# Performance work log

Measured on AMD Instinct MI355X. Metric: run time of the kernel, lower is better.

The kernel has to match this reference:

```python
import jax, jax.numpy as jnp
import numpy as np

B, L, D, H = 2, 2048, 1024, 16
DH = D // H  # per-head dim = 64


def setup_inputs() -> dict:
    key = jax.random.key(0)
    ks = jax.random.split(key, 7)
    s = 1.0 / np.sqrt(D)
    x = jax.random.normal(ks[0], (B, L, D), dtype=jnp.float32)
    Wq = jax.random.normal(ks[1], (D, D), dtype=jnp.float32) * s
    bq = jax.random.normal(ks[2], (D,), dtype=jnp.float32) * s
    Wk = jax.random.normal(ks[3], (D, D), dtype=jnp.float32) * s
    bk = jax.random.normal(ks[4], (D,), dtype=jnp.float32) * s
    Wv = jax.random.normal(ks[5], (D, D), dtype=jnp.float32) * s
    bv = jax.random.normal(ks[6], (D,), dtype=jnp.float32) * s
    # strict upper-triangular causal mask; mask==1 means position is masked (-inf)
    atten_mask = jnp.triu(jnp.ones((L, L), dtype=jnp.int32), k=1)
    return {"x": x, "atten_mask": atten_mask, "Wq": Wq, "bq": bq,
            "Wk": Wk, "bk": bk, "Wv": Wv, "bv": bv}


def reference(x, atten_mask, Wq, bq, Wk, bk, Wv, bv):
    # nn.Linear: y = x @ W^T + b
    q = x @ Wq.T + bq  # [B,L,D]
    k = x @ Wk.T + bk
    v = x @ Wv.T + bv
    # contiguous split into heads == reshape to [B,L,H,DH]
    q = q.reshape(B, L, H, DH)
    k = k.reshape(B, L, H, DH)
    v = v.reshape(B, L, H, DH)
    scale = jnp.sqrt(jnp.float32(DH))
    scores = jnp.einsum('blhd,bmhd->bhlm', q, k) / scale  # [B,H,L,L]
    # torch.where(mask == 1, -inf, scores)
    scores = jnp.where(atten_mask[None, None] == 1, -jnp.inf, scores)
    attn = jax.nn.softmax(scores, axis=-1)
    out = jnp.einsum('bhlm,bmhd->blhd', attn, v)  # [B,L,H,DH]
    return out.reshape(B, L, D)  # concat heads along channel dim
```

## Files before the change

kernel.cpp:

```cpp
#include <hip/hip_runtime.h>
#include <hip/hip_bf16.h>

#define BDIM 2
#define LSEQ 2048
#define DMODEL 1024
#define NH 16
#define DHEAD 64
#define CTS 136

typedef __bf16 bf16_t;
typedef __attribute__((ext_vector_type(8))) __bf16 bf16x8;
typedef __attribute__((ext_vector_type(4))) __bf16 bf16x4;
typedef __attribute__((ext_vector_type(2))) __bf16 bf16x2;
typedef __attribute__((ext_vector_type(4))) float f32x4;
typedef __attribute__((ext_vector_type(4))) int i32x4;

static __device__ __forceinline__ f32x4 mfma16(bf16x8 a, bf16x8 b, f32x4 c) {
    return __builtin_amdgcn_mfma_f32_16x16x32_bf16(a, b, c, 0, 0, 0);
}

static __device__ __forceinline__ void load_lds16(const bf16_t* g, void* l) {
    __builtin_amdgcn_global_load_lds(
        (const __attribute__((address_space(1))) void*)g,
        (__attribute__((address_space(3))) void*)l, 16, 0, 0);
}

__global__ void convert_all(
    const float* __restrict__ x,
    const float* __restrict__ Wq, const float* __restrict__ Wk, const float* __restrict__ Wv,
    const float* __restrict__ bq, const float* __restrict__ bk, const float* __restrict__ bv,
    bf16_t* __restrict__ cx,
    bf16_t* __restrict__ cWq, bf16_t* __restrict__ cWk, bf16_t* __restrict__ cWv,
    bf16_t* __restrict__ cbq, bf16_t* __restrict__ cbk, bf16_t* __restrict__ cbv,
    float SQ)
{
    const int blk = blockIdx.x;
    const float* src; bf16_t* dst; int base, cnt; float sc = 1.0f;
    if (blk < 1024)      { src = x;  dst = cx;  base = blk * 1024;          cnt = 1024; }
    else if (blk < 1280) { src = Wq; dst = cWq; base = (blk - 1024) * 1024; cnt = 1024; sc = SQ; }
    else if (blk < 1536) { src = Wk; dst = cWk; base = (blk - 1280) * 1024; cnt = 1024; }
    else if (blk < 1792) { src = Wv; dst = cWv; base = (blk - 1536) * 1024; cnt = 1024; }
    else if (blk == 1792){ src = bq; dst = cbq; base = 0; cnt = 256; sc = SQ; }
    else if (blk == 1793){ src = bk; dst = cbk; base = 0; cnt = 256; }
    else                 { src = bv; dst = cbv; base = 0; cnt = 256; }

    for (int i = base + threadIdx.x; i < base + cnt; i += 256) {
        f32x4 v = *(const f32x4*)(src + 4 * (size_t)i);
        bf16x4 o;
        o[0] = (bf16_t)(v[0] * sc); o[1] = (bf16_t)(v[1] * sc);
        o[2] = (bf16_t)(v[2] * sc); o[3] = (bf16_t)(v[3] * sc);
        *(bf16x4*)(dst + 4 * (size_t)i) = o;
    }
}

__global__ __launch_bounds__(256) void qkv_gemm(
    const bf16_t* __restrict__ x,
    const bf16_t* __restrict__ W0, const bf16_t* __restrict__ W1, const bf16_t* __restrict__ W2,
    const bf16_t* __restrict__ b0, const bf16_t* __restrict__ b1, const bf16_t* __restrict__ b2,
    bf16_t* __restrict__ yq, bf16_t* __restrict__ yk, bf16_t* __restrict__ yvT)
{
    __shared__ alignas(16) char smem[128 * CTS * 2];
    bf16_t* At = (bf16_t*)smem;
    bf16_t* Bt = At + 128 * 64;
    bf16_t* Ct = (bf16_t*)smem;

    const int tid  = threadIdx.x;
    const int lane = tid & 63;
    const int w    = tid >> 6;
    const int quad = lane >> 4;
    const int n16  = lane & 15;
    const int lane3 = lane >> 3;
    const int lane7 = lane & 7;
    const int swz8  = (lane7 ^ lane3) * 8;

    const int m0 = blockIdx.y * 128;
    const int n0 = blockIdx.x * 128;
    const int z  = blockIdx.z;

    const bf16_t* W    = (z == 0) ? W0 : ((z == 1) ? W1 : W2);
    const bf16_t* bias = (z == 0) ? b0 : ((z == 1) ? b1 : b2);

    const int wm = (w >> 1) * 64;
    const int wn = (w & 1) * 64;

    f32x4 acc[4][4] = {};

    const bf16_t* gx = x + (size_t)(m0 + 32 * w + lane3) * DMODEL + swz8;
    const bf16_t* gw = W + (size_t)(n0 + 32 * w + lane3) * DMODEL + swz8;
    char* lA = (char*)At + w * 4096;
    char* lB = (char*)Bt + w * 4096;

    const int swz = n16 & 7;

    for (int k0 = 0; k0 < DMODEL; k0 += 64) {
        #pragma unroll
        for (int ii = 0; ii < 4; ++ii) {
            load_lds16(gx + (size_t)(8 * ii) * DMODEL + k0, lA + ii * 1024);
            load_lds16(gw + (size_t)(8 * ii) * DMODEL + k0, lB + ii * 1024);
        }
        __syncthreads();

        #pragma unroll
        for (int kk = 0; kk < 2; ++kk) {
            bf16x8 af[4], bfv[4];
            #pragma unroll
            for (int mt = 0; mt < 4; ++mt) {
                const bf16_t* ar = At + (wm + mt * 16 + n16) * 64;
                af[mt] = *(const bf16x8*)(ar + (((quad + 4 * kk)) ^ swz) * 8);
            }
            #pragma unroll
            for (int nt = 0; nt < 4; ++nt) {
                const bf16_t* br = Bt + (wn + nt * 16 + n16) * 64;
                bfv[nt] = *(const bf16x8*)(br + (((quad + 4 * kk)) ^ swz) * 8);
            }
            #pragma unroll
            for (int mt = 0; mt < 4; ++mt)
                #pragma unroll
                for (int nt = 0; nt < 4; ++nt)
                    acc[mt][nt] = mfma16(af[mt], bfv[nt], acc[mt][nt]);
        }
        __syncthreads();
    }

    if (z < 2) {
        bf16_t* y = (z == 0) ? yq : yk;
        #pragma unroll
        for (int nt = 0; nt < 4; ++nt) {
            int jc = wn + nt * 16 + n16;
            float bv = (float)bias[n0 + jc];
            #pragma unroll
            for (int mt = 0; mt < 4; ++mt) {
                int rr = wm + mt * 16 + quad * 4;
                #pragma unroll
                for (int r = 0; r < 4; ++r)
                    Ct[(rr + r) * CTS + jc] = (bf16_t)(acc[mt][nt][r] + bv);
            }
        }
        __syncthreads();
        const int l    = tid >> 1;
        const int half = tid & 1;
        const int hh   = (n0 >> 6) + half;
        const int i    = m0 + l;
        const int bb   = i >> 11, ll = i & 2047;
        bf16_t* dst = &y[(((size_t)bb * NH + hh) * LSEQ + ll) * DHEAD];
        const bf16_t* srcr = &Ct[l * CTS + half * 64];
        #pragma unroll
        for (int c = 0; c < 8; ++c)
            *(bf16x8*)(dst + c * 8) = *(const bf16x8*)(srcr + c * 8);
    } else {
        #pragma unroll
        for (int nt = 0; nt < 4; ++nt) {
            int j = n0 + wn + nt * 16 + n16;
            float bv = (float)bias[j];
            #pragma unroll
            for (int mt = 0; mt < 4; ++mt) {
                int i0 = m0 + wm + mt * 16 + quad * 4;
                int bb = i0 >> 11, l = i0 & 2047;
                bf16x4 pk;
                #pragma unroll
                for (int r = 0; r < 4; ++r) pk[r] = (bf16_t)(acc[mt][nt][r] + bv);
                *(bf16x4*)(&yvT[((size_t)bb * DMODEL + j) * LSEQ + l]) = pk;
            }
        }
    }
}

__global__ __launch_bounds__(256) void attn_fused(
    const bf16_t* __restrict__ qp,
    const bf16_t* __restrict__ kp,
    const bf16_t* __restrict__ vtp,
    float* __restrict__ out,
    float* __restrict__ Opart,
    float* __restrict__ ml)
{
    __shared__ alignas(16) bf16_t Ks[2][64 * 64];
    __shared__ alignas(16) bf16_t Vs[2][64 * 64];

    const int tid  = threadIdx.x;
    const int lane = tid & 63;
    const int w    = tid >> 6;
    const int quad = lane >> 4;
    const int n16  = lane & 15;
    const int lane3 = lane >> 3;
    const int lane7 = lane & 7;
    const int swz8  = (lane7 ^ lane3) * 8;
    const int swz   = n16 & 7;

    const int bh  = blockIdx.x;
    const int yy  = blockIdx.y;
    const int p   = yy & 7;
    const bool isA = (yy < 8);
    const int b = bh >> 4, h = bh & 15;
    const size_t hb = (size_t)bh * (LSEQ * DHEAD);

    float l_[2];
    f32x4 oacc[2][4];

    auto process = [&](int qt, int t0, int ntiles, bool maskTail) {
        int iqg[2];
        bf16x8 qb[2][2];
        #pragma unroll
        for (int g = 0; g < 2; ++g) {
            iqg[g] = qt * 128 + 32 * w + 16 * g + n16;
            const bf16_t* qq = qp + hb + (size_t)iqg[g] * DHEAD;
            qb[g][0] = *(const bf16x8*)(qq + quad * 8);
            qb[g][1] = *(const bf16x8*)(qq + 32 + quad * 8);
        }

        const bf16_t* gk = kp  + hb + (size_t)(t0 * 64 + 16 * w + lane3) * DHEAD + swz8;
        const bf16_t* gv = vtp + hb + (size_t)(16 * w + lane3) * LSEQ + t0 * 64 + swz8;

        int buf = 0;
        {
            char* lk = (char*)&Ks[0][0] + w * 2048;
            char* lv = (char*)&Vs[0][0] + w * 2048;
            load_lds16(gk,             lk);
            load_lds16(gk + 8 * DHEAD, lk + 1024);
            load_lds16(gv,             lv);
            load_lds16(gv + 8 * LSEQ,  lv + 1024);
            gk += 64 * DHEAD; gv += 64;
        }
        __syncthreads();

        for (int it = 0; it < ntiles; ++it) {
            if (it + 1 < ntiles) {
                char* lk = (char*)&Ks[buf ^ 1][0] + w * 2048;
                char* lv = (char*)&Vs[buf ^ 1][0] + w * 2048;
                load_lds16(gk,             lk);
                load_lds16(gk + 8 * DHEAD, lk + 1024);
                load_lds16(gv,             lv);
                load_lds16(gv + 8 * LSEQ,  lv + 1024);
                gk += 64 * DHEAD; gv += 64;
            }

            const bf16_t* kb = &Ks[buf][0];
            f32x4 s[2][4];
            #pragma unroll
            for (int t = 0; t < 4; ++t) {
                const bf16_t* krow = kb + (t * 16 + n16) * 64;
                bf16x8 k0v = *(const bf16x8*)(krow + ((quad    ) ^ swz) * 8);
                bf16x8 k1v = *(const bf16x8*)(krow + ((quad + 4) ^ swz) * 8);
                #pragma unroll
                for (int g = 0; g < 2; ++g) {
                    f32x4 z = {0.f, 0.f, 0.f, 0.f};
                    z = mfma16(k0v, qb[g][0], z);
                    z = mfma16(k1v, qb[g][1], z);
                    s[g][t] = z;
                }
            }

            if (maskTail && it >= ntiles - 2) {
                const int k0 = (t0 + it) * 64;
                #pragma unroll
                for (int g = 0; g < 2; ++g)
                    #pragma unroll
                    for (int t = 0; t < 4; ++t)
                        #pragma unroll
                        for (int r = 0; r < 4; ++r)
                            if (k0 + t * 16 + quad * 4 + r > iqg[g]) s[g][t][r] = -1e30f;
            }

            bf16x8 pb[2][2];
            #pragma unroll
            for (int g = 0; g < 2; ++g) {
                float rs = 0.f;
                int pr[4][2];
                #pragma unroll
                for (int t = 0; t < 4; ++t) {
                    float p0 = __builtin_amdgcn_exp2f(s[g][t][0]);
                    float p1 = __builtin_amdgcn_exp2f(s[g][t][1]);
                    float p2 = __builtin_amdgcn_exp2f(s[g][t][2]);
                    float p3 = __builtin_amdgcn_exp2f(s[g][t][3]);
                    rs += (p0 + p1) + (p2 + p3);
                    bf16x2 a; a[0] = (bf16_t)p0; a[1] = (bf16_t)p1;
                    bf16x2 c; c[0] = (bf16_t)p2; c[1] = (bf16_t)p3;
                    pr[t][0] = __builtin_bit_cast(int, a);
                    pr[t][1] = __builtin_bit_cast(int, c);
                }
                l_[g] += rs;

                #pragma unroll
                for (int c = 0; c < 2; ++c) {
                    int frag[4];
                    #pragma unroll
                    for (int pi = 0; pi < 4; ++pi) {
                        int srcl = ((((quad & 1) * 2) + (pi >> 1)) * 16 + n16) * 4;
                        int vA = __builtin_amdgcn_ds_bpermute(srcl, pr[2 * c][pi & 1]);
                        int vB = __builtin_amdgcn_ds_bpermute(srcl, pr[2 * c + 1][pi & 1]);
                        frag[pi] = (quad < 2) ? vA : vB;
                    }
                    i32x4 fv = {frag[0], frag[1], frag[2], frag[3]};
                    pb[g][c] = __builtin_bit_cast(bf16x8, fv);
                }
            }

            const bf16_t* vbs = &Vs[buf][0];
            #pragma unroll
            for (int c = 0; c < 2; ++c) {
                #pragma unroll
                for (int t = 0; t < 4; ++t) {
                    const bf16_t* vrow = vbs + (t * 16 + n16) * 64;
                    bf16x8 va = *(const bf16x8*)(vrow + ((quad + 4 * c) ^ swz) * 8);
                    oacc[0][t] = mfma16(va, pb[0][c], oacc[0][t]);
                    oacc[1][t] = mfma16(va, pb[1][c], oacc[1][t]);
                }
            }

            __syncthreads();
            buf ^= 1;
        }
    };

    auto zero_state = [&]() {
        #pragma unroll
        for (int g = 0; g < 2; ++g) {
            l_[g] = 0.f;
            #pragma unroll
            for (int t = 0; t < 4; ++t) { f32x4 zz = {0.f,0.f,0.f,0.f}; oacc[g][t] = zz; }
        }
    };

    auto store_partial = [&](int pidx) {
        #pragma unroll
        for (int g = 0; g < 2; ++g) {
            float ls = l_[g];
            ls += __shfl_xor(ls, 16, 64);
            ls += __shfl_xor(ls, 32, 64);
            const int row = 32 * w + 16 * g + n16;
            float* Ob = Opart + (size_t)pidx * (128 * 64) + row * 64;
            #pragma unroll
            for (int t = 0; t < 4; ++t)
                *(f32x4*)(Ob + t * 16 + quad * 4) = oacc[g][t];
            if (quad == 0) ml[(size_t)pidx * 128 + row] = ls;
        }
    };

    if (isA) {
        zero_state();
        process(p, 0, 2 * p + 2, true);
        #pragma unroll
        for (int g = 0; g < 2; ++g) {
            float ls = l_[g];
            ls += __shfl_xor(ls, 16, 64);
            ls += __shfl_xor(ls, 32, 64);
            const float inv = 1.0f / ls;
            const int iq = p * 128 + 32 * w + 16 * g + n16;
            float* orow = out + ((size_t)b * LSEQ + iq) * DMODEL + h * DHEAD;
            #pragma unroll
            for (int t = 0; t < 4; ++t) {
                f32x4 o;
                o[0] = oacc[g][t][0] * inv; o[1] = oacc[g][t][1] * inv;
                o[2] = oacc[g][t][2] * inv; o[3] = oacc[g][t][3] * inv;
                *(f32x4*)(orow + t * 16 + quad * 4) = o;
            }
        }
        zero_state();
        process(15 - p, 0, 15 - 2 * p, false);
        store_partial((bh * 8 + (7 - p)) * 2 + 0);
    } else {
        zero_state();
        process(15 - p, 15 - 2 * p, 17, true);
        store_partial((bh * 8 + (7 - p)) * 2 + 1);
    }
}

__global__ __launch_bounds__(256) void attn_combine(
    const float* __restrict__ Opart, const float* __restrict__ ml,
    float* __restrict__ out)
{
    const int bh = blockIdx.x;
    const int q8 = blockIdx.y;
    const int t  = threadIdx.x;
    const int row = t >> 1;
    const int dh0 = (t & 1) * 32;
    const int p0  = (bh * 8 + q8) * 2;
    const int b = bh >> 4, h = bh & 15;

    float l0 = ml[(size_t)p0 * 128 + row];
    float l1 = ml[(size_t)(p0 + 1) * 128 + row];
    float inv = 1.0f / (l0 + l1);

    const float* P0 = Opart + (size_t)p0 * (128 * 64) + row * 64 + dh0;
    const float* P1 = P0 + 128 * 64;
    float* orow = out + ((size_t)b * LSEQ + ((8 + q8) * 128 + row)) * DMODEL
                + h * DHEAD + dh0;
    #pragma unroll
    for (int c = 0; c < 8; ++c) {
        f32x4 o0 = *(const f32x4*)(P0 + 4 * c);
        f32x4 o1 = *(const f32x4*)(P1 + 4 * c);
        f32x4 o;
        o[0] = (o0[0] + o1[0]) * inv;
        o[1] = (o0[1] + o1[1]) * inv;
        o[2] = (o0[2] + o1[2]) * inv;
        o[3] = (o0[3] + o1[3]) * inv;
        *(f32x4*)(orow + 4 * c) = o;
    }
}

extern "C" void kernel_launch(void* const* d_in, const int* in_sizes, int n_in,
                              void* d_out, int out_size, void* d_ws, size_t ws_size,
                              hipStream_t stream)
{
    const float* x  = (const float*)d_in[0];
    const float* Wq = (const float*)d_in[2];
    const float* bq = (const float*)d_in[3];
    const float* Wk = (const float*)d_in[4];
    const float* bk = (const float*)d_in[5];
    const float* Wv = (const float*)d_in[6];
    const float* bv = (const float*)d_in[7];
    float* out = (float*)d_out;

    char* ws = (char*)d_ws;
    bf16_t* q   = (bf16_t*)(ws);
    bf16_t* k   = (bf16_t*)(ws + 8u  * 1024 * 1024);
    bf16_t* vT  = (bf16_t*)(ws + 16u * 1024 * 1024);
    bf16_t* cx  = (bf16_t*)(ws + 24u * 1024 * 1024);
    bf16_t* cWq = (bf16_t*)(ws + 32u * 1024 * 1024);
    bf16_t* cWk = (bf16_t*)(ws + 34u * 1024 * 1024);
    bf16_t* cWv = (bf16_t*)(ws + 36u * 1024 * 1024);
    bf16_t* cbq = (bf16_t*)(ws + 38u * 1024 * 1024);
    bf16_t* cbk = (bf16_t*)(ws + 38u * 1024 * 1024 + 4096);
    bf16_t* cbv = (bf16_t*)(ws + 38u * 1024 * 1024 + 8192);
    float*  mlp = (float*) (ws + 39u * 1024 * 1024);
    float*  Op  = (float*) (ws + 40u * 1024 * 1024);

    const float SQ = 0.125f * 1.44269504088896f;

    convert_all<<<1795, 256, 0, stream>>>(x, Wq, Wk, Wv, bq, bk, bv,
                                          cx, cWq, cWk, cWv, cbq, cbk, cbv, SQ);

    dim3 g1(DMODEL / 128, (BDIM * LSEQ) / 128, 3);
    qkv_gemm<<<g1, 256, 0, stream>>>(cx, cWq, cWk, cWv, cbq, cbk, cbv, q, k, vT);

    dim3 g2(BDIM * NH, 16, 1);
    attn_fused<<<g2, 256, 0, stream>>>(q, k, vT, out, Op, mlp);

    dim3 g3(BDIM * NH, 8, 1);
    attn_combine<<<g3, 256, 0, stream>>>(Op, mlp, out);
}
```

Baseline: 188.1 us.

## Rebalance causal attention into 30 table-driven split-KV jobs per head

Replaces the paired A/B block scheme (16 blocks per head, some running two passes) with a static job table of 30 blocks per head. Each block handles one query tile over a KV range of at most about 12 tiles, and longer query tiles are split into 2 or 3 partials. The combine kernel now sums a variable number of partials per query tile. The goal is shorter, more even per-block work and more blocks to fill the CUs. The cost is extra partial writes and reads and a moved workspace layout, where the Op buffer now overlaps the cx region.

```diff
diff --git a/kernel.cpp b/kernel.cpp
--- a/kernel.cpp
+++ b/kernel.cpp
@@ -173,6 +173,17 @@
     float* __restrict__ Opart,
     float* __restrict__ ml)
 {
+    static const short JQT[30] = {0,1,2,3,4,5, 6,6, 7,7, 8,8, 9,9, 10,10, 11,11,
+                                  12,12,12, 13,13,13, 14,14,14, 15,15,15};
+    static const short JT0[30] = {0,0,0,0,0,0, 0,7, 0,8, 0,9, 0,10, 0,11, 0,12,
+                                  0,9,18, 0,10,19, 0,10,20, 0,11,22};
+    static const short JNT[30] = {2,4,6,8,10,12, 7,7, 8,8, 9,9, 10,10, 11,11, 12,12,
+                                  9,9,8, 10,9,9, 10,10,10, 11,11,10};
+    static const short JPS[30] = {-1,-1,-1,-1,-1,-1, 0,1, 2,3, 4,5, 6,7, 8,9, 10,11,
+                                  12,13,14, 15,16,17, 18,19,20, 21,22,23};
+    static const short JMK[30] = {1,1,1,1,1,1, 0,1, 0,1, 0,1, 0,1, 0,1, 0,1,
+                                  0,0,1, 0,0,1, 0,0,1, 0,0,1};
+
     __shared__ alignas(16) bf16_t Ks[2][64 * 64];
     __shared__ alignas(16) bf16_t Vs[2][64 * 64];
 
@@ -187,140 +198,150 @@
     const int swz   = n16 & 7;
 
     const int bh  = blockIdx.x;
-    const int yy  = blockIdx.y;
-    const int p   = yy & 7;
-    const bool isA = (yy < 8);
+    const int job = blockIdx.y;
+    const int qt     = JQT[job];
+    const int t0     = JT0[job];
+    const int ntiles = JNT[job];
+    const int pslot  = JPS[job];
+    const bool maskTail = (JMK[job] != 0);
+
     const int b = bh >> 4, h = bh & 15;
     const size_t hb = (size_t)bh * (LSEQ * DHEAD);
 
-    float l_[2];
-    f32x4 oacc[2][4];
-
-    auto process = [&](int qt, int t0, int ntiles, bool maskTail) {
-        int iqg[2];
-        bf16x8 qb[2][2];
-        #pragma unroll
-        for (int g = 0; g < 2; ++g) {
-            iqg[g] = qt * 128 + 32 * w + 16 * g + n16;
-            const bf16_t* qq = qp + hb + (size_t)iqg[g] * DHEAD;
-            qb[g][0] = *(const bf16x8*)(qq + quad * 8);
-            qb[g][1] = *(const bf16x8*)(qq + 32 + quad * 8);
-        }
-
-        const bf16_t* gk = kp  + hb + (size_t)(t0 * 64 + 16 * w + lane3) * DHEAD + swz8;
-        const bf16_t* gv = vtp + hb + (size_t)(16 * w + lane3) * LSEQ + t0 * 64 + swz8;
-
-        int buf = 0;
-        {
-            char* lk = (char*)&Ks[0][0] + w * 2048;
-            char* lv = (char*)&Vs[0][0] + w * 2048;
+    float l_[2] = {0.f, 0.f};
+    f32x4 oacc[2][4] = {};
+
+    int iqg[2];
+    bf16x8 qb[2][2];
+    #pragma unroll
+    for (int g = 0; g < 2; ++g) {
+        iqg[g] = qt * 128 + 32 * w + 16 * g + n16;
+        const bf16_t* qq = qp + hb + (size_t)iqg[g] * DHEAD;
+        qb[g][0] = *(const bf16x8*)(qq + quad * 8);
+        qb[g][1] = *(const bf16x8*)(qq + 32 + quad * 8);
+    }
+
+    const bf16_t* gk = kp  + hb + (size_t)(t0 * 64 + 16 * w + lane3) * DHEAD + swz8;
+    const bf16_t* gv = vtp + hb + (size_t)(16 * w + lane3) * LSEQ + t0 * 64 + swz8;
+
+    int buf = 0;
+    {
+        char* lk = (char*)&Ks[0][0] + w * 2048;
+        char* lv = (char*)&Vs[0][0] + w * 2048;
+        load_lds16(gk,             lk);
+        load_lds16(gk + 8 * DHEAD, lk + 1024);
+        load_lds16(gv,             lv);
+        load_lds16(gv + 8 * LSEQ,  lv + 1024);
+        gk += 64 * DHEAD; gv += 64;
+    }
+    __syncthreads();
+
+    for (int it = 0; it < ntiles; ++it) {
+        if (it + 1 < ntiles) {
+            char* lk = (char*)&Ks[buf ^ 1][0] + w * 2048;
+            char* lv = (char*)&Vs[buf ^ 1][0] + w * 2048;
             load_lds16(gk,             lk);
             load_lds16(gk + 8 * DHEAD, lk + 1024);
             load_lds16(gv,             lv);
             load_lds16(gv + 8 * LSEQ,  lv + 1024);
             gk += 64 * DHEAD; gv += 64;
         }
+
+        const bf16_t* kb = &Ks[buf][0];
+        f32x4 s[2][4];
+        #pragma unroll
+        for (int t = 0; t < 4; ++t) {
+            const bf16_t* krow = kb + (t * 16 + n16) * 64;
+            bf16x8 k0v = *(const bf16x8*)(krow + ((quad    ) ^ swz) * 8);
+            bf16x8 k1v = *(const bf16x8*)(krow + ((quad + 4) ^ swz) * 8);
+            #pragma unroll
+            for (int g = 0; g < 2; ++g) {
+                f32x4 z = {0.f, 0.f, 0.f, 0.f};
+                z = mfma16(k0v, qb[g][0], z);
+                z = mfma16(k1v, qb[g][1], z);
+                s[g][t] = z;
+            }
+        }
+
+        if (maskTail && it >= ntiles - 2) {
+            const int k0 = (t0 + it) * 64;
+            #pragma unroll
+            for (int g = 0; g < 2; ++g)
+                #pragma unroll
+                for (int t = 0; t < 4; ++t)
+                    #pragma unroll
+                    for (int r = 0; r < 4; ++r)
+                        if (k0 + t * 16 + quad * 4 + r > iqg[g]) s[g][t][r] = -1e30f;
+        }
+
+        bf16x8 pb[2][2];
+        #pragma unroll
+        for (int g = 0; g < 2; ++g) {
+            float rs = 0.f;
+            int pr[4][2];
+            #pragma unroll
+            for (int t = 0; t < 4; ++t) {
+                float p0 = __builtin_amdgcn_exp2f(s[g][t][0]);
+                float p1 = __builtin_amdgcn_exp2f(s[g][t][1]);
+                float p2 = __builtin_amdgcn_exp2f(s[g][t][2]);
+                float p3 = __builtin_amdgcn_exp2f(s[g][t][3]);
+                rs += (p0 + p1) + (p2 + p3);
+                bf16x2 a; a[0] = (bf16_t)p0; a[1] = (bf16_t)p1;
+                bf16x2 c; c[0] = (bf16_t)p2; c[1] = (bf16_t)p3;
+                pr[t][0] = __builtin_bit_cast(int, a);
+                pr[t][1] = __builtin_bit_cast(int, c);
+            }
+            l_[g] += rs;
+
+            #pragma unroll
+            for (int c = 0; c < 2; ++c) {
+                int frag[4];
+                #pragma unroll
+                for (int pi = 0; pi < 4; ++pi) {
+                    int srcl = ((((quad & 1) * 2) + (pi >> 1)) * 16 + n16) * 4;
+                    int vA = __builtin_amdgcn_ds_bpermute(srcl, pr[2 * c][pi & 1]);
+                    int vB = __builtin_amdgcn_ds_bpermute(srcl, pr[2 * c + 1][pi & 1]);
+                    frag[pi] = (quad < 2) ? vA : vB;
+                }
+                i32x4 fv = {frag[0], frag[1], frag[2], frag[3]};
+                pb[g][c] = __builtin_bit_cast(bf16x8, fv);
+            }
+        }
+
+        const bf16_t* vbs = &Vs[buf][0];
+        #pragma unroll
+        for (int c = 0; c < 2; ++c) {
+            #pragma unroll
+            for (int t = 0; t < 4; ++t) {
+                const bf16_t* vrow = vbs + (t * 16 + n16) * 64;
+                bf16x8 va = *(const bf16x8*)(vrow + ((quad + 4 * c) ^ swz) * 8);
+                oacc[0][t] = mfma16(va, pb[0][c], oacc[0][t]);
+                oacc[1][t] = mfma16(va, pb[1][c], oacc[1][t]);
+            }
+        }
+
         __syncthreads();
-
-        for (int it = 0; it < ntiles; ++it) {
-            if (it + 1 < ntiles) {
-                char* lk = (char*)&Ks[buf ^ 1][0] + w * 2048;
-                char* lv = (char*)&Vs[buf ^ 1][0] + w * 2048;
-                load_lds16(gk,             lk);
-                load_lds16(gk + 8 * DHEAD, lk + 1024);
-                load_lds16(gv,             lv);
-                load_lds16(gv + 8 * LSEQ,  lv + 1024);
-                gk += 64 * DHEAD; gv += 64;
-            }
-
-            const bf16_t* kb = &Ks[buf][0];
-            f32x4 s[2][4];
+        buf ^= 1;
+    }
+
+    if (pslot < 0) {
+        #pragma unroll
+        for (int g = 0; g < 2; ++g) {
+            float ls = l_[g];
+            ls += __shfl_xor(ls, 16, 64);
+            ls += __shfl_xor(ls, 32, 64);
+            const float inv = 1.0f / ls;
+            float* orow = out + ((size_t)b * LSEQ + iqg[g]) * DMODEL + h * DHEAD;
             #pragma unroll
             for (int t = 0; t < 4; ++t) {
-                const bf16_t* krow = kb + (t * 16 + n16) * 64;
-                bf16x8 k0v = *(const bf16x8*)(krow + ((quad    ) ^ swz) * 8);
-                bf16x8 k1v = *(const bf16x8*)(krow + ((quad + 4) ^ swz) * 8);
-                #pragma unroll
-                for (int g = 0; g < 2; ++g) {
-                    f32x4 z = {0.f, 0.f, 0.f, 0.f};
-                    z = mfma16(k0v, qb[g][0], z);
-                    z = mfma16(k1v, qb[g][1], z);
-                    s[g][t] = z;
-                }
-            }
-
-            if (maskTail && it >= ntiles - 2) {
-                const int k0 = (t0 + it) * 64;
-                #pragma unroll
-                for (int g = 0; g < 2; ++g)
-                    #pragma unroll
-                    for (int t = 0; t < 4; ++t)
-                        #pragma unroll
-                        for (int r = 0; r < 4; ++r)
-                            if (k0 + t * 16 + quad * 4 + r > iqg[g]) s[g][t][r] = -1e30f;
-            }
-
-            bf16x8 pb[2][2];
-            #pragma unroll
-            for (int g = 0; g < 2; ++g) {
-                float rs = 0.f;
-                int pr[4][2];
-                #pragma unroll
-                for (int t = 0; t < 4; ++t) {
-                    float p0 = __builtin_amdgcn_exp2f(s[g][t][0]);
-                    float p1 = __builtin_amdgcn_exp2f(s[g][t][1]);
-                    float p2 = __builtin_amdgcn_exp2f(s[g][t][2]);
-                    float p3 = __builtin_amdgcn_exp2f(s[g][t][3]);
-                    rs += (p0 + p1) + (p2 + p3);
-                    bf16x2 a; a[0] = (bf16_t)p0; a[1] = (bf16_t)p1;
-                    bf16x2 c; c[0] = (bf16_t)p2; c[1] = (bf16_t)p3;
-                    pr[t][0] = __builtin_bit_cast(int, a);
-                    pr[t][1] = __builtin_bit_cast(int, c);
-                }
-                l_[g] += rs;
-
-                #pragma unroll
-                for (int c = 0; c < 2; ++c) {
-                    int frag[4];
-                    #pragma unroll
-                    for (int pi = 0; pi < 4; ++pi) {
-                        int srcl = ((((quad & 1) * 2) + (pi >> 1)) * 16 + n16) * 4;
-                        int vA = __builtin_amdgcn_ds_bpermute(srcl, pr[2 * c][pi & 1]);
-                        int vB = __builtin_amdgcn_ds_bpermute(srcl, pr[2 * c + 1][pi & 1]);
-                        frag[pi] = (quad < 2) ? vA : vB;
-                    }
-                    i32x4 fv = {frag[0], frag[1], frag[2], frag[3]};
-                    pb[g][c] = __builtin_bit_cast(bf16x8, fv);
-                }
-            }
-
-            const bf16_t* vbs = &Vs[buf][0];
-            #pragma unroll
-            for (int c = 0; c < 2; ++c) {
-                #pragma unroll
-                for (int t = 0; t < 4; ++t) {
-                    const bf16_t* vrow = vbs + (t * 16 + n16) * 64;
-                    bf16x8 va = *(const bf16x8*)(vrow + ((quad + 4 * c) ^ swz) * 8);
-                    oacc[0][t] = mfma16(va, pb[0][c], oacc[0][t]);
-                    oacc[1][t] = mfma16(va, pb[1][c], oacc[1][t]);
-                }
-            }
-
-            __syncthreads();
-            buf ^= 1;
-        }
-    };
-
-    auto zero_state = [&]() {
-        #pragma unroll
-        for (int g = 0; g < 2; ++g) {
-            l_[g] = 0.f;
-            #pragma unroll
-            for (int t = 0; t < 4; ++t) { f32x4 zz = {0.f,0.f,0.f,0.f}; oacc[g][t] = zz; }
-        }
-    };
-
-    auto store_partial = [&](int pidx) {
+                f32x4 o;
+                o[0] = oacc[g][t][0] * inv; o[1] = oacc[g][t][1] * inv;
+                o[2] = oacc[g][t][2] * inv; o[3] = oacc[g][t][3] * inv;
+                *(f32x4*)(orow + t * 16 + quad * 4) = o;
+            }
+        }
+    } else {
+        const int pidx = bh * 24 + pslot;
         #pragma unroll
         for (int g = 0; g < 2; ++g) {
             float ls = l_[g];
@@ -333,34 +354,6 @@
                 *(f32x4*)(Ob + t * 16 + quad * 4) = oacc[g][t];
             if (quad == 0) ml[(size_t)pidx * 128 + row] = ls;
         }
-    };
-
-    if (isA) {
-        zero_state();
-        process(p, 0, 2 * p + 2, true);
-        #pragma unroll
-        for (int g = 0; g < 2; ++g) {
-            float ls = l_[g];
-            ls += __shfl_xor(ls, 16, 64);
-            ls += __shfl_xor(ls, 32, 64);
-            const float inv = 1.0f / ls;
-            const int iq = p * 128 + 32 * w + 16 * g + n16;
-            float* orow = out + ((size_t)b * LSEQ + iq) * DMODEL + h * DHEAD;
-            #pragma unroll
-            for (int t = 0; t < 4; ++t) {
-                f32x4 o;
-                o[0] = oacc[g][t][0] * inv; o[1] = oacc[g][t][1] * inv;
-                o[2] = oacc[g][t][2] * inv; o[3] = oacc[g][t][3] * inv;
-                *(f32x4*)(orow + t * 16 + quad * 4) = o;
-            }
-        }
-        zero_state();
-        process(15 - p, 0, 15 - 2 * p, false);
-        store_partial((bh * 8 + (7 - p)) * 2 + 0);
-    } else {
-        zero_state();
-        process(15 - p, 15 - 2 * p, 17, true);
-        store_partial((bh * 8 + (7 - p)) * 2 + 1);
     }
 }
 
@@ -368,31 +361,35 @@
     const float* __restrict__ Opart, const float* __restrict__ ml,
     float* __restrict__ out)
 {
+    static const short PB[10] = {0,2,4,6,8,10, 12,15,18,21};
+    static const short PK[10] = {2,2,2,2,2,2, 3,3,3,3};
+
     const int bh = blockIdx.x;
-    const int q8 = blockIdx.y;
+    const int y  = blockIdx.y;
     const int t  = threadIdx.x;
     const int row = t >> 1;
     const int dh0 = (t & 1) * 32;
-    const int p0  = (bh * 8 + q8) * 2;
+    const int k    = PK[y];
+    const int p0   = bh * 24 + PB[y];
     const int b = bh >> 4, h = bh & 15;
 
-    float l0 = ml[(size_t)p0 * 128 + row];
-    float l1 = ml[(size_t)(p0 + 1) * 128 + row];
-    float inv = 1.0f / (l0 + l1);
-
-    const float* P0 = Opart + (size_t)p0 * (128 * 64) + row * 64 + dh0;
-    const float* P1 = P0 + 128 * 64;
-    float* orow = out + ((size_t)b * LSEQ + ((8 + q8) * 128 + row)) * DMODEL
+    float lsum = 0.f;
+    for (int i = 0; i < k; ++i) lsum += ml[(size_t)(p0 + i) * 128 + row];
+    const float inv = 1.0f / lsum;
+
+    float* orow = out + ((size_t)b * LSEQ + ((6 + y) * 128 + row)) * DMODEL
                 + h * DHEAD + dh0;
     #pragma unroll
     for (int c = 0; c < 8; ++c) {
-        f32x4 o0 = *(const f32x4*)(P0 + 4 * c);
-        f32x4 o1 = *(const f32x4*)(P1 + 4 * c);
+        f32x4 acc = {0.f, 0.f, 0.f, 0.f};
+        for (int i = 0; i < k; ++i) {
+            const float* P = Opart + (size_t)(p0 + i) * (128 * 64) + row * 64 + dh0;
+            f32x4 o = *(const f32x4*)(P + 4 * c);
+            acc[0] += o[0]; acc[1] += o[1]; acc[2] += o[2]; acc[3] += o[3];
+        }
         f32x4 o;
-        o[0] = (o0[0] + o1[0]) * inv;
-        o[1] = (o0[1] + o1[1]) * inv;
-        o[2] = (o0[2] + o1[2]) * inv;
-        o[3] = (o0[3] + o1[3]) * inv;
+        o[0] = acc[0] * inv; o[1] = acc[1] * inv;
+        o[2] = acc[2] * inv; o[3] = acc[3] * inv;
         *(f32x4*)(orow + 4 * c) = o;
     }
 }
@@ -421,8 +418,8 @@
     bf16_t* cbq = (bf16_t*)(ws + 38u * 1024 * 1024);
     bf16_t* cbk = (bf16_t*)(ws + 38u * 1024 * 1024 + 4096);
     bf16_t* cbv = (bf16_t*)(ws + 38u * 1024 * 1024 + 8192);
-    float*  mlp = (float*) (ws + 39u * 1024 * 1024);
-    float*  Op  = (float*) (ws + 40u * 1024 * 1024);
+    float*  Op  = (float*) (ws + 24u * 1024 * 1024);
+    float*  mlp = (float*) (ws + 48u * 1024 * 1024);
 
     const float SQ = 0.125f * 1.44269504088896f;
 
@@ -432,9 +429,9 @@
     dim3 g1(DMODEL / 128, (BDIM * LSEQ) / 128, 3);
     qkv_gemm<<<g1, 256, 0, stream>>>(cx, cWq, cWk, cWv, cbq, cbk, cbv, q, k, vT);
 
-    dim3 g2(BDIM * NH, 16, 1);
+    dim3 g2(BDIM * NH, 30, 1);
     attn_fused<<<g2, 256, 0, stream>>>(q, k, vT, out, Op, mlp);
 
-    dim3 g3(BDIM * NH, 8, 1);
+    dim3 g3(BDIM * NH, 10, 1);
     attn_combine<<<g3, 256, 0, stream>>>(Op, mlp, out);
 }
```

Result: slower. 200.3 us (+6.5%).

## Double-buffer QKV GEMM LDS tiles with K=32 steps to overlap loads

Applied to the files above, without the earlier changes.

The QKV projection GEMM now uses two LDS buffers with a K-step of 32 instead of a single buffer with a K-step of 64. The next tile's global-to-LDS loads are issued before computing on the current tile, and the XOR swizzle is changed to suit 32-wide rows. The goal is to overlap global memory latency with MFMA work and remove one barrier per iteration. In exchange it runs twice as many iterations, each with less compute to hide latency behind.

```diff
diff --git a/kernel.cpp b/kernel.cpp
--- a/kernel.cpp
+++ b/kernel.cpp
@@ -59,19 +59,14 @@
     const bf16_t* __restrict__ b0, const bf16_t* __restrict__ b1, const bf16_t* __restrict__ b2,
     bf16_t* __restrict__ yq, bf16_t* __restrict__ yk, bf16_t* __restrict__ yvT)
 {
-    __shared__ alignas(16) char smem[128 * CTS * 2];
-    bf16_t* At = (bf16_t*)smem;
-    bf16_t* Bt = At + 128 * 64;
-    bf16_t* Ct = (bf16_t*)smem;
+    __shared__ alignas(16) bf16_t smem[128 * CTS];
+    bf16_t* Ct = smem;
 
     const int tid  = threadIdx.x;
     const int lane = tid & 63;
     const int w    = tid >> 6;
     const int quad = lane >> 4;
     const int n16  = lane & 15;
-    const int lane3 = lane >> 3;
-    const int lane7 = lane & 7;
-    const int swz8  = (lane7 ^ lane3) * 8;
 
     const int m0 = blockIdx.y * 128;
     const int n0 = blockIdx.x * 128;
@@ -85,41 +80,57 @@
 
     f32x4 acc[4][4] = {};
 
-    const bf16_t* gx = x + (size_t)(m0 + 32 * w + lane3) * DMODEL + swz8;
-    const bf16_t* gw = W + (size_t)(n0 + 32 * w + lane3) * DMODEL + swz8;
-    char* lA = (char*)At + w * 4096;
-    char* lB = (char*)Bt + w * 4096;
-
-    const int swz = n16 & 7;
-
-    for (int k0 = 0; k0 < DMODEL; k0 += 64) {
-        #pragma unroll
-        for (int ii = 0; ii < 4; ++ii) {
-            load_lds16(gx + (size_t)(8 * ii) * DMODEL + k0, lA + ii * 1024);
-            load_lds16(gw + (size_t)(8 * ii) * DMODEL + k0, lB + ii * 1024);
-        }
+    const int srow  = lane >> 2;
+    const int schnk = (lane & 3) ^ (srow & 3);
+    const bf16_t* gx = x + (size_t)(m0 + w * 32 + srow) * DMODEL + schnk * 8;
+    const bf16_t* gw = W + (size_t)(n0 + w * 32 + srow) * DMODEL + schnk * 8;
+    const int ldsOff = w * 1024;
+
+    const int rswz = n16 & 3;
+
+    {
+        bf16_t* lA = smem + ldsOff;
+        bf16_t* lB = smem + 4096 + ldsOff;
+        load_lds16(gx,               lA);
+        load_lds16(gx + 16 * DMODEL, lA + 512);
+        load_lds16(gw,               lB);
+        load_lds16(gw + 16 * DMODEL, lB + 512);
+    }
+    __syncthreads();
+
+    int buf = 0;
+    for (int it = 0; it < DMODEL / 32; ++it) {
+        if (it + 1 < DMODEL / 32) {
+            const int k0 = (it + 1) * 32;
+            bf16_t* lA = smem + (buf ^ 1) * 8192 + ldsOff;
+            bf16_t* lB = smem + (buf ^ 1) * 8192 + 4096 + ldsOff;
+            load_lds16(gx + k0,               lA);
+            load_lds16(gx + 16 * DMODEL + k0, lA + 512);
+            load_lds16(gw + k0,               lB);
+            load_lds16(gw + 16 * DMODEL + k0, lB + 512);
+        }
+
+        const bf16_t* Ab = smem + buf * 8192;
+        const bf16_t* Bb = smem + buf * 8192 + 4096;
+        bf16x8 af[4], bfv[4];
+        #pragma unroll
+        for (int mt = 0; mt < 4; ++mt) {
+            const bf16_t* ar = Ab + (wm + mt * 16 + n16) * 32;
+            af[mt] = *(const bf16x8*)(ar + (quad ^ rswz) * 8);
+        }
+        #pragma unroll
+        for (int nt = 0; nt < 4; ++nt) {
+            const bf16_t* br = Bb + (wn + nt * 16 + n16) * 32;
+            bfv[nt] = *(const bf16x8*)(br + (quad ^ rswz) * 8);
+        }
+        #pragma unroll
+        for (int mt = 0; mt < 4; ++mt)
+            #pragma unroll
+            for (int nt = 0; nt < 4; ++nt)
+                acc[mt][nt] = mfma16(af[mt], bfv[nt], acc[mt][nt]);
+
         __syncthreads();
-
-        #pragma unroll
-        for (int kk = 0; kk < 2; ++kk) {
-            bf16x8 af[4], bfv[4];
-            #pragma unroll
-            for (int mt = 0; mt < 4; ++mt) {
-                const bf16_t* ar = At + (wm + mt * 16 + n16) * 64;
-                af[mt] = *(const bf16x8*)(ar + (((quad + 4 * kk)) ^ swz) * 8);
-            }
-            #pragma unroll
-            for (int nt = 0; nt < 4; ++nt) {
-                const bf16_t* br = Bt + (wn + nt * 16 + n16) * 64;
-                bfv[nt] = *(const bf16x8*)(br + (((quad + 4 * kk)) ^ swz) * 8);
-            }
-            #pragma unroll
-            for (int mt = 0; mt < 4; ++mt)
-                #pragma unroll
-                for (int nt = 0; nt < 4; ++nt)
-                    acc[mt][nt] = mfma16(af[mt], bfv[nt], acc[mt][nt]);
-        }
-        __syncthreads();
+        buf ^= 1;
     }
 
     if (z < 2) {
```

New measurement: 191.4 us. Within noise of the previous version (+1.8%).
